# Optimization experiments

Measured on AMD Instinct MI355X. Metric: run time of the kernel, lower is better.

## Reference

```python
import jax, jax.numpy as jnp
import numpy as np


def setup_inputs() -> dict:
    key = jax.random.key(0)
    feature = jax.random.normal(key, (32, 64, 128, 128), dtype=jnp.float32)
    return {"feature": feature}


def reference(feature):
    # feature: [B, C, H, W]
    B, C, H, W = feature.shape
    mgr = feature.mean()  # global mean over all elements

    # Per-(sample, channel) argmax location; row-major first-occurrence matches
    # the original strict '>' scan.
    flat_idx = jnp.argmax(feature.reshape(B, C, H * W), axis=-1)  # [B, C]
    max_x = flat_idx // W  # row index
    max_y = flat_idx % W   # col index

    i = jnp.arange(H)
    j = jnp.arange(W)
    # squared distance from each pixel to its channel's argmax: [B, C, H, W]
    dist2 = ((max_x[:, :, None, None] - i[None, None, :, None]) ** 2
             + (max_y[:, :, None, None] - j[None, None, None, :]) ** 2)
    dist2 = dist2.astype(feature.dtype)

    f2 = feature * feature
    dis_loss = jnp.sum(f2 * dist2)

    # max over OTHER channels at each pixel: top-2 over channel axis,
    # use 2nd max only for the channel that is the (first) argmax.
    t = jnp.moveaxis(feature, 1, -1)  # [B, H, W, C]
    top2, _ = jax.lax.top_k(t, 2)    # [B, H, W, 2]
    m1 = top2[..., 0][:, None, :, :]  # [B, 1, H, W]
    m2 = top2[..., 1][:, None, :, :]
    amax_c = jnp.argmax(t, axis=-1)[:, None, :, :]  # [B, 1, H, W]
    c_ids = jnp.arange(C)[None, :, None, None]      # [1, C, 1, 1]
    max_others = jnp.where(c_ids == amax_c, m2, m1)  # [B, C, H, W]

    div_loss = jnp.sum(f2 * (max_others - mgr) ** 2)

    n = B * C * H * W
    return dis_loss / n, div_loss / n
```

## Files before the change

### kernel.cpp

```cpp
#include <hip/hip_runtime.h>

#define HW    16384
#define WDIM  128
#define CDIM  64
#define BDIM  32
#define NB1   (BDIM * CDIM)
#define NB2   ((BDIM * HW) / 512)


__global__ __launch_bounds__(256) void k1_channel(const float* __restrict__ feat,
                                                  double* __restrict__ ws) {
    const int t = threadIdx.x;
    const size_t base = (size_t)blockIdx.x * HW;
    const float4* f4 = (const float4*)(feat + base);

    float4 buf[16];
    #pragma unroll
    for (int k = 0; k < 16; ++k) buf[k] = f4[t + k * 256];

    float best = -INFINITY; int bidx = 0;
    float sf = 0.f, s0 = 0.f, si = 0.f, sj = 0.f, sq = 0.f;
    #pragma unroll
    for (int k = 0; k < 16; ++k) {
        int p = t + k * 256;
        int e = p * 4;
        int i  = e >> 7;
        int jb = e & 127;
        float x0 = buf[k].x, x1 = buf[k].y, x2 = buf[k].z, x3 = buf[k].w;
        if (x0 > best) { best = x0; bidx = e;     }
        if (x1 > best) { best = x1; bidx = e + 1; }
        if (x2 > best) { best = x2; bidx = e + 2; }
        if (x3 > best) { best = x3; bidx = e + 3; }
        float q0 = x0*x0, q1 = x1*x1, q2 = x2*x2, q3 = x3*x3;
        float qs = q0 + q1 + q2 + q3;
        sf += x0 + x1 + x2 + x3;
        s0 += qs;
        si += qs * (float)i;
        sj += q0*(float)jb + q1*(float)(jb+1) + q2*(float)(jb+2) + q3*(float)(jb+3);
        float ii = (float)(i * i);
        sq += q0*(ii + (float)( jb   * jb   ))
            + q1*(ii + (float)((jb+1)*(jb+1)))
            + q2*(ii + (float)((jb+2)*(jb+2)))
            + q3*(ii + (float)((jb+3)*(jb+3)));
    }

    __shared__ float smax[256]; __shared__ int sidx[256];
    __shared__ float rf[256], r0[256], ri[256], rj[256], rq[256];
    smax[t] = best; sidx[t] = bidx;
    rf[t] = sf; r0[t] = s0; ri[t] = si; rj[t] = sj; rq[t] = sq;
    __syncthreads();

    for (int off = 128; off > 0; off >>= 1) {
        if (t < off) {
            float vo = smax[t + off]; int io = sidx[t + off];
            if (vo > smax[t] || (vo == smax[t] && io < sidx[t])) { smax[t] = vo; sidx[t] = io; }
            rf[t] += rf[t + off]; r0[t] += r0[t + off];
            ri[t] += ri[t + off]; rj[t] += rj[t + off]; rq[t] += rq[t + off];
        }
        __syncthreads();
    }

    if (t == 0) {
        int mi = sidx[0] >> 7, mj = sidx[0] & 127;
        double T0 = r0[0], TI = ri[0], TJ = rj[0], TQ = rq[0];
        double dis = (double)(mi*mi + mj*mj) * T0 + TQ - 2.0*mi*TI - 2.0*mj*TJ;
        ws[blockIdx.x]        = (double)rf[0];
        ws[2048 + blockIdx.x] = T0;
        ws[4096 + blockIdx.x] = dis;
    }
}

__global__ __launch_bounds__(256) void k2_pixel(const float* __restrict__ feat,
                                                double* __restrict__ ws) {
    const int t = threadIdx.x;
    const int pp = blockIdx.x * 256 + t;
    const int b   = pp >> 13;
    const int hw2 = pp & 8191;
    const float2* src = (const float2*)(feat + (size_t)b * CDIM * HW) + hw2;

    float2 v[CDIM];
    #pragma unroll
    for (int c = 0; c < CDIM; ++c) v[c] = src[c * (HW / 2)];

    float m1x = -INFINITY, m2x = -INFINITY; int i1x = 0;
    float m1y = -INFINITY, m2y = -INFINITY; int i1y = 0;
    #pragma unroll
    for (int c = 0; c < CDIM; ++c) {
        float x = v[c].x, y = v[c].y;
        if (x > m1x)      { m2x = m1x; m1x = x; i1x = c; }
        else if (x > m2x) { m2x = x; }
        if (y > m1y)      { m2y = m1y; m1y = y; i1y = c; }
        else if (y > m2y) { m2y = y; }
    }

    float a1 = 0.f, a2 = 0.f;
    #pragma unroll
    for (int c = 0; c < CDIM; ++c) {
        float x = v[c].x, y = v[c].y;
        float f2x = x * x, f2y = y * y;
        float mox = (c == i1x) ? m2x : m1x;
        float moy = (c == i1y) ? m2y : m1y;
        a1 += f2x * mox * mox + f2y * moy * moy;
        a2 += f2x * mox + f2y * moy;
    }

    __shared__ float r1[256], r2[256];
    r1[t] = a1; r2[t] = a2;
    __syncthreads();
    for (int off = 128; off > 0; off >>= 1) {
        if (t < off) { r1[t] += r1[t + off]; r2[t] += r2[t + off]; }
        __syncthreads();
    }
    if (t == 0) {
        ws[6144 + blockIdx.x] = (double)r1[0];
        ws[7168 + blockIdx.x] = (double)r2[0];
    }
}

__global__ __launch_bounds__(256) void k3_final(const double* __restrict__ ws,
                                                float* __restrict__ out) {
    const int t = threadIdx.x;
    double sf = 0, s0 = 0, dis = 0, a1 = 0, a2 = 0;
    for (int i = t; i < 2048; i += 256) {
        sf  += ws[i];
        s0  += ws[2048 + i];
        dis += ws[4096 + i];
    }
    for (int i = t; i < 1024; i += 256) {
        a1 += ws[6144 + i];
        a2 += ws[7168 + i];
    }
    __shared__ double r[5][256];
    r[0][t] = sf; r[1][t] = s0; r[2][t] = dis; r[3][t] = a1; r[4][t] = a2;
    __syncthreads();
    for (int off = 128; off > 0; off >>= 1) {
        if (t < off) {
            #pragma unroll
            for (int q = 0; q < 5; ++q) r[q][t] += r[q][t + off];
        }
        __syncthreads();
    }
    if (t == 0) {
        const double n = 33554432.0;
        double mgr = r[0][0] / n;
        out[0] = (float)(r[2][0] / n);
        out[1] = (float)((r[3][0] - 2.0 * mgr * r[4][0] + mgr * mgr * r[1][0]) / n);
    }
}

extern "C" void kernel_launch(void* const* d_in, const int* in_sizes, int n_in,
                              void* d_out, int out_size, void* d_ws, size_t ws_size,
                              hipStream_t stream) {
    const float* feat = (const float*)d_in[0];
    float* out = (float*)d_out;
    double* ws = (double*)d_ws;

    k1_channel<<<NB1, 256, 0, stream>>>(feat, ws);
    k2_pixel<<<NB2, 256, 0, stream>>>(feat, ws);
    k3_final<<<1, 256, 0, stream>>>(ws, out);
}
```

Baseline: 65.27 us.

## Stream pixel pass with float4 and closed-form div-loss from top-2 and sum of squares

The per-pixel kernel no longer buffers all 64 channel values in registers and makes a second pass. It streams float4 loads once, tracking the top-2 value and the sum of squares for each pixel. The div-loss terms then come in closed form: the argmax channel uses m2, and every other channel uses m1 weighted by (sum of squares minus m1 squared). This removes the 64-entry register array and the second loop, and halves the block count. The risk is float cancellation in s2 - m1^2.

Measured after the change: 58.91 us. 9.7% less time.

```diff
diff --git a/kernel.cpp b/kernel.cpp
--- a/kernel.cpp
+++ b/kernel.cpp
@@ -5,7 +5,7 @@
 #define CDIM  64
 #define BDIM  32
 #define NB1   (BDIM * CDIM)
-#define NB2   ((BDIM * HW) / 512)
+#define NB2   ((BDIM * HW) / 1024)
 
 
 __global__ __launch_bounds__(256) void k1_channel(const float* __restrict__ feat,
@@ -73,35 +73,41 @@
 __global__ __launch_bounds__(256) void k2_pixel(const float* __restrict__ feat,
                                                 double* __restrict__ ws) {
     const int t = threadIdx.x;
-    const int pp = blockIdx.x * 256 + t;
-    const int b   = pp >> 13;
-    const int hw2 = pp & 8191;
-    const float2* src = (const float2*)(feat + (size_t)b * CDIM * HW) + hw2;
+    const int p4 = blockIdx.x * 256 + t;
+    const int b   = p4 >> 12;
+    const int hw4 = p4 & 4095;
+    const float4* src = (const float4*)(feat + (size_t)b * CDIM * HW) + hw4;
 
-    float2 v[CDIM];
-    #pragma unroll
-    for (int c = 0; c < CDIM; ++c) v[c] = src[c * (HW / 2)];
+    float m1x=-INFINITY, m2x=-INFINITY, s2x=0.f;
+    float m1y=-INFINITY, m2y=-INFINITY, s2y=0.f;
+    float m1z=-INFINITY, m2z=-INFINITY, s2z=0.f;
+    float m1w=-INFINITY, m2w=-INFINITY, s2w=0.f;
 
-    float m1x = -INFINITY, m2x = -INFINITY; int i1x = 0;
-    float m1y = -INFINITY, m2y = -INFINITY; int i1y = 0;
     #pragma unroll
     for (int c = 0; c < CDIM; ++c) {
-        float x = v[c].x, y = v[c].y;
-        if (x > m1x)      { m2x = m1x; m1x = x; i1x = c; }
-        else if (x > m2x) { m2x = x; }
-        if (y > m1y)      { m2y = m1y; m1y = y; i1y = c; }
-        else if (y > m2y) { m2y = y; }
+        float4 v = src[c * (HW / 4)];
+        if (v.x > m1x) { m2x = m1x; m1x = v.x; } else { m2x = fmaxf(m2x, v.x); }
+        if (v.y > m1y) { m2y = m1y; m1y = v.y; } else { m2y = fmaxf(m2y, v.y); }
+        if (v.z > m1z) { m2z = m1z; m1z = v.z; } else { m2z = fmaxf(m2z, v.z); }
+        if (v.w > m1w) { m2w = m1w; m1w = v.w; } else { m2w = fmaxf(m2w, v.w); }
+        s2x = fmaf(v.x, v.x, s2x);
+        s2y = fmaf(v.y, v.y, s2y);
+        s2z = fmaf(v.z, v.z, s2z);
+        s2w = fmaf(v.w, v.w, s2w);
     }
 
-    float a1 = 0.f, a2 = 0.f;
-    #pragma unroll
-    for (int c = 0; c < CDIM; ++c) {
-        float x = v[c].x, y = v[c].y;
-        float f2x = x * x, f2y = y * y;
-        float mox = (c == i1x) ? m2x : m1x;
-        float moy = (c == i1y) ? m2y : m1y;
-        a1 += f2x * mox * mox + f2y * moy * moy;
-        a2 += f2x * mox + f2y * moy;
+    float a1, a2;
+    {
+        float qx = m1x*m1x, qy = m1y*m1y, qz = m1z*m1z, qw = m1w*m1w;
+        float rx = s2x - qx, ry = s2y - qy, rz = s2z - qz, rw = s2w - qw;
+        a1 = qx*rx + m2x*m2x*qx
+           + qy*ry + m2y*m2y*qy
+           + qz*rz + m2z*m2z*qz
+           + qw*rw + m2w*m2w*qw;
+        a2 = m1x*rx + m2x*qx
+           + m1y*ry + m2y*qy
+           + m1z*rz + m2z*qz
+           + m1w*rw + m2w*qw;
     }
 
     __shared__ float r1[256], r2[256];
@@ -112,8 +118,8 @@
         __syncthreads();
     }
     if (t == 0) {
-        ws[6144 + blockIdx.x] = (double)r1[0];
-        ws[7168 + blockIdx.x] = (double)r2[0];
+        ws[6144 + blockIdx.x]       = (double)r1[0];
+        ws[6144 + NB2 + blockIdx.x] = (double)r2[0];
     }
 }
 
@@ -121,14 +127,14 @@
                                                 float* __restrict__ out) {
     const int t = threadIdx.x;
     double sf = 0, s0 = 0, dis = 0, a1 = 0, a2 = 0;
-    for (int i = t; i < 2048; i += 256) {
+    for (int i = t; i < NB1; i += 256) {
         sf  += ws[i];
         s0  += ws[2048 + i];
         dis += ws[4096 + i];
     }
-    for (int i = t; i < 1024; i += 256) {
+    for (int i = t; i < NB2; i += 256) {
         a1 += ws[6144 + i];
-        a2 += ws[7168 + i];
+        a2 += ws[6144 + NB2 + i];
     }
     __shared__ double r[5][256];
     r[0][t] = sf; r[1][t] = s0; r[2][t] = dis; r[3][t] = a1; r[4][t] = a2;
```

## Fuse channel and pixel passes into one row-tiled kernel via shared memory

Applied to the files above, without the earlier changes.

Replaces the separate per-channel and per-pixel passes, which each read the whole tensor, with one kernel that loads a (batch,row) slab of all channels into LDS and computes both the top-2 divergence terms and per-channel row partials. A second small kernel reduces the row partials per channel to find the argmax and the distance loss. The divergence term is rewritten algebraically so it no longer needs the per-pixel argmax channel index. This halves global memory reads at the cost of an extra kernel launch and more workspace traffic.

Measured after the change: 54.97 us (median of 2 runs). -15.8%, faster.

```diff
diff --git a/kernel.cpp b/kernel.cpp
--- a/kernel.cpp
+++ b/kernel.cpp
@@ -1,135 +1,180 @@
 #include <hip/hip_runtime.h>
 
-#define HW    16384
-#define WDIM  128
-#define CDIM  64
-#define BDIM  32
-#define NB1   (BDIM * CDIM)
-#define NB2   ((BDIM * HW) / 512)
-
-
-__global__ __launch_bounds__(256) void k1_channel(const float* __restrict__ feat,
-                                                  double* __restrict__ ws) {
+#define HW     16384
+#define WDIM   128
+#define HDIM   128
+#define CDIM   64
+#define BDIM   32
+#define CHUNKS 128
+#define NBF    (BDIM * CHUNKS)
+#define NBC    (BDIM * CDIM)
+
+
+#define OFF_WMAX  0
+#define OFF_WIDX  (1u << 20)
+#define OFF_WSF   (2u << 20)
+#define OFF_WS0   (3u << 20)
+#define OFF_WSJ   (4u << 20)
+#define OFF_WSQJ  (5u << 20)
+#define OFF_WA1   (6u << 20)
+#define OFF_WA2   ((6u << 20) + 32768u)
+#define OFF_K3    ((6u << 20) + 65536u)
+
+__global__ __launch_bounds__(256) void f_fused(const float* __restrict__ feat,
+                                               float* __restrict__ wmax, int* __restrict__ widx,
+                                               float* __restrict__ wsf,  float* __restrict__ ws0,
+                                               float* __restrict__ wsj,  float* __restrict__ wsqj,
+                                               double* __restrict__ wa1, double* __restrict__ wa2) {
+    __shared__ float tile[CDIM * 129];
+    __shared__ float sc2[128 * 3];
+    __shared__ float ared[128 * 2];
+    __shared__ float scb[4 * 64 * 7];
+
+    const int t  = threadIdx.x;
+    const int bf = blockIdx.x;
+    const int b  = bf >> 7, row = bf & 127;
+    const float* src = feat + (size_t)b * CDIM * HW + (size_t)row * WDIM;
+
+    float4 buf[8];
+    #pragma unroll
+    for (int k = 0; k < 8; ++k) {
+        int idx = k * 256 + t;
+        int c = idx >> 5, g = idx & 31;
+        buf[k] = *(const float4*)(src + (size_t)c * HW + g * 4);
+    }
+    #pragma unroll
+    for (int k = 0; k < 8; ++k) {
+        int idx = k * 256 + t;
+        int c = idx >> 5, g = idx & 31;
+        float* dst = &tile[c * 129 + g * 4];
+        dst[0] = buf[k].x; dst[1] = buf[k].y; dst[2] = buf[k].z; dst[3] = buf[k].w;
+    }
+    __syncthreads();
+
+    {
+        const int px = t & 127, half = t >> 7;
+        float m1 = -INFINITY, m2 = -INFINITY, s2 = 0.f;
+        #pragma unroll
+        for (int cc = 0; cc < 32; ++cc) {
+            float x = tile[(half * 32 + cc) * 129 + px];
+            if (x > m1) { m2 = m1; m1 = x; } else { m2 = fmaxf(m2, x); }
+            s2 = fmaf(x, x, s2);
+        }
+        if (half) { sc2[px * 3] = m1; sc2[px * 3 + 1] = m2; sc2[px * 3 + 2] = s2; }
+        __syncthreads();
+        if (!half) {
+            float n1 = sc2[px * 3], n2 = sc2[px * 3 + 1], s2b = sc2[px * 3 + 2];
+            float mm1 = fmaxf(m1, n1);
+            float mm2 = fmaxf(fminf(m1, n1), fmaxf(m2, n2));
+            float S2 = s2 + s2b;
+            float q = mm1 * mm1, r = S2 - q;
+            ared[px * 2]     = q * r + mm2 * mm2 * q;
+            ared[px * 2 + 1] = mm1 * r + mm2 * q;
+        }
+        __syncthreads();
+        for (int off = 64; off > 0; off >>= 1) {
+            if (t < off) {
+                ared[t * 2]     += ared[(t + off) * 2];
+                ared[t * 2 + 1] += ared[(t + off) * 2 + 1];
+            }
+            __syncthreads();
+        }
+        if (t == 0) { wa1[bf] = (double)ared[0]; wa2[bf] = (double)ared[1]; }
+    }
+
+    {
+        const int ch = t & 63, sub = t >> 6;
+        const int p0 = sub * 32;
+        float bm = -INFINITY; int bpx = 0;
+        float sf = 0.f, s0 = 0.f, sj = 0.f, sqj = 0.f;
+        #pragma unroll
+        for (int i = 0; i < 32; ++i) {
+            int p = p0 + i;
+            float x = tile[ch * 129 + p];
+            if (x > bm) { bm = x; bpx = p; }
+            sf += x;
+            float q = x * x;
+            s0 += q;
+            sj  = fmaf(q, (float)p, sj);
+            sqj = fmaf(q, (float)(p * p), sqj);
+        }
+        int o = (sub * 64 + ch) * 7;
+        scb[o] = bm; scb[o + 1] = __int_as_float(bpx);
+        scb[o + 2] = sf; scb[o + 3] = s0; scb[o + 4] = sj; scb[o + 5] = sqj;
+        __syncthreads();
+        if (t < 64) {
+            float M = -INFINITY; int P = 0;
+            float SF = 0.f, S0 = 0.f, SJ = 0.f, SQ = 0.f;
+            #pragma unroll
+            for (int s = 0; s < 4; ++s) {
+                int oo = (s * 64 + t) * 7;
+                float m = scb[oo];
+                if (m > M) { M = m; P = __float_as_int(scb[oo + 1]); }
+                SF += scb[oo + 2]; S0 += scb[oo + 3];
+                SJ += scb[oo + 4]; SQ += scb[oo + 5];
+            }
+            int out = bf * 64 + t;
+            wmax[out] = M; widx[out] = P;
+            wsf[out] = SF; ws0[out] = S0; wsj[out] = SJ; wsqj[out] = SQ;
+        }
+    }
+}
+
+__global__ __launch_bounds__(128) void k3_channel(const float* __restrict__ wmax, const int* __restrict__ widx,
+                                                  const float* __restrict__ wsf,  const float* __restrict__ ws0,
+                                                  const float* __restrict__ wsj,  const float* __restrict__ wsqj,
+                                                  double* __restrict__ k3out) {
+    const int bc = blockIdx.x;
+    const int b = bc >> 6, c = bc & 63;
     const int t = threadIdx.x;
-    const size_t base = (size_t)blockIdx.x * HW;
-    const float4* f4 = (const float4*)(feat + base);
-
-    float4 buf[16];
-    #pragma unroll
-    for (int k = 0; k < 16; ++k) buf[k] = f4[t + k * 256];
-
-    float best = -INFINITY; int bidx = 0;
-    float sf = 0.f, s0 = 0.f, si = 0.f, sj = 0.f, sq = 0.f;
-    #pragma unroll
-    for (int k = 0; k < 16; ++k) {
-        int p = t + k * 256;
-        int e = p * 4;
-        int i  = e >> 7;
-        int jb = e & 127;
-        float x0 = buf[k].x, x1 = buf[k].y, x2 = buf[k].z, x3 = buf[k].w;
-        if (x0 > best) { best = x0; bidx = e;     }
-        if (x1 > best) { best = x1; bidx = e + 1; }
-        if (x2 > best) { best = x2; bidx = e + 2; }
-        if (x3 > best) { best = x3; bidx = e + 3; }
-        float q0 = x0*x0, q1 = x1*x1, q2 = x2*x2, q3 = x3*x3;
-        float qs = q0 + q1 + q2 + q3;
-        sf += x0 + x1 + x2 + x3;
-        s0 += qs;
-        si += qs * (float)i;
-        sj += q0*(float)jb + q1*(float)(jb+1) + q2*(float)(jb+2) + q3*(float)(jb+3);
-        float ii = (float)(i * i);
-        sq += q0*(ii + (float)( jb   * jb   ))
-            + q1*(ii + (float)((jb+1)*(jb+1)))
-            + q2*(ii + (float)((jb+2)*(jb+2)))
-            + q3*(ii + (float)((jb+3)*(jb+3)));
-    }
-
-    __shared__ float smax[256]; __shared__ int sidx[256];
-    __shared__ float rf[256], r0[256], ri[256], rj[256], rq[256];
-    smax[t] = best; sidx[t] = bidx;
-    rf[t] = sf; r0[t] = s0; ri[t] = si; rj[t] = sj; rq[t] = sq;
-    __syncthreads();
-
-    for (int off = 128; off > 0; off >>= 1) {
+    const int idx = (b * 128 + t) * 64 + c;
+
+    float m = wmax[idx]; int px = widx[idx];
+    float sf = wsf[idx], s0 = ws0[idx], sj = wsj[idx], sqj = wsqj[idx];
+
+    __shared__ float rm[128]; __shared__ int rr[128]; __shared__ int rp[128];
+    rm[t] = m; rr[t] = t; rp[t] = px;
+    __syncthreads();
+    for (int off = 64; off > 0; off >>= 1) {
         if (t < off) {
-            float vo = smax[t + off]; int io = sidx[t + off];
-            if (vo > smax[t] || (vo == smax[t] && io < sidx[t])) { smax[t] = vo; sidx[t] = io; }
-            rf[t] += rf[t + off]; r0[t] += r0[t + off];
-            ri[t] += ri[t + off]; rj[t] += rj[t + off]; rq[t] += rq[t + off];
-        }
-        __syncthreads();
-    }
-
+            float mo = rm[t + off];
+            if (mo > rm[t] || (mo == rm[t] && rr[t + off] < rr[t])) {
+                rm[t] = mo; rr[t] = rr[t + off]; rp[t] = rp[t + off];
+            }
+        }
+        __syncthreads();
+    }
+    const int mi = rr[0], mj = rp[0];
+
+    double di = (double)(mi - t);
+    double disc = (di * di + (double)mj * (double)mj) * (double)s0
+                - 2.0 * (double)mj * (double)sj + (double)sqj;
+
+    __shared__ double rd[128], rsf[128], rs0[128];
+    rd[t] = disc; rsf[t] = (double)sf; rs0[t] = (double)s0;
+    __syncthreads();
+    for (int off = 64; off > 0; off >>= 1) {
+        if (t < off) { rd[t] += rd[t + off]; rsf[t] += rsf[t + off]; rs0[t] += rs0[t + off]; }
+        __syncthreads();
+    }
     if (t == 0) {
-        int mi = sidx[0] >> 7, mj = sidx[0] & 127;
-        double T0 = r0[0], TI = ri[0], TJ = rj[0], TQ = rq[0];
-        double dis = (double)(mi*mi + mj*mj) * T0 + TQ - 2.0*mi*TI - 2.0*mj*TJ;
-        ws[blockIdx.x]        = (double)rf[0];
-        ws[2048 + blockIdx.x] = T0;
-        ws[4096 + blockIdx.x] = dis;
-    }
-}
-
-__global__ __launch_bounds__(256) void k2_pixel(const float* __restrict__ feat,
-                                                double* __restrict__ ws) {
-    const int t = threadIdx.x;
-    const int pp = blockIdx.x * 256 + t;
-    const int b   = pp >> 13;
-    const int hw2 = pp & 8191;
-    const float2* src = (const float2*)(feat + (size_t)b * CDIM * HW) + hw2;
-
-    float2 v[CDIM];
-    #pragma unroll
-    for (int c = 0; c < CDIM; ++c) v[c] = src[c * (HW / 2)];
-
-    float m1x = -INFINITY, m2x = -INFINITY; int i1x = 0;
-    float m1y = -INFINITY, m2y = -INFINITY; int i1y = 0;
-    #pragma unroll
-    for (int c = 0; c < CDIM; ++c) {
-        float x = v[c].x, y = v[c].y;
-        if (x > m1x)      { m2x = m1x; m1x = x; i1x = c; }
-        else if (x > m2x) { m2x = x; }
-        if (y > m1y)      { m2y = m1y; m1y = y; i1y = c; }
-        else if (y > m2y) { m2y = y; }
-    }
-
-    float a1 = 0.f, a2 = 0.f;
-    #pragma unroll
-    for (int c = 0; c < CDIM; ++c) {
-        float x = v[c].x, y = v[c].y;
-        float f2x = x * x, f2y = y * y;
-        float mox = (c == i1x) ? m2x : m1x;
-        float moy = (c == i1y) ? m2y : m1y;
-        a1 += f2x * mox * mox + f2y * moy * moy;
-        a2 += f2x * mox + f2y * moy;
-    }
-
-    __shared__ float r1[256], r2[256];
-    r1[t] = a1; r2[t] = a2;
-    __syncthreads();
-    for (int off = 128; off > 0; off >>= 1) {
-        if (t < off) { r1[t] += r1[t + off]; r2[t] += r2[t + off]; }
-        __syncthreads();
-    }
-    if (t == 0) {
-        ws[6144 + blockIdx.x] = (double)r1[0];
-        ws[7168 + blockIdx.x] = (double)r2[0];
-    }
-}
-
-__global__ __launch_bounds__(256) void k3_final(const double* __restrict__ ws,
+        k3out[bc * 3]     = rsf[0];
+        k3out[bc * 3 + 1] = rs0[0];
+        k3out[bc * 3 + 2] = rd[0];
+    }
+}
+
+__global__ __launch_bounds__(256) void k4_final(const double* __restrict__ k3out,
+                                                const double* __restrict__ wa1,
+                                                const double* __restrict__ wa2,
                                                 float* __restrict__ out) {
     const int t = threadIdx.x;
     double sf = 0, s0 = 0, dis = 0, a1 = 0, a2 = 0;
-    for (int i = t; i < 2048; i += 256) {
-        sf  += ws[i];
-        s0  += ws[2048 + i];
-        dis += ws[4096 + i];
-    }
-    for (int i = t; i < 1024; i += 256) {
-        a1 += ws[6144 + i];
-        a2 += ws[7168 + i];
-    }
+    for (int i = t; i < NBC; i += 256) {
+        sf += k3out[i * 3]; s0 += k3out[i * 3 + 1]; dis += k3out[i * 3 + 2];
+    }
+    for (int i = t; i < NBF; i += 256) { a1 += wa1[i]; a2 += wa2[i]; }
+
     __shared__ double r[5][256];
     r[0][t] = sf; r[1][t] = s0; r[2][t] = dis; r[3][t] = a1; r[4][t] = a2;
     __syncthreads();
@@ -153,9 +198,19 @@
                               hipStream_t stream) {
     const float* feat = (const float*)d_in[0];
     float* out = (float*)d_out;
-    double* ws = (double*)d_ws;
-
-    k1_channel<<<NB1, 256, 0, stream>>>(feat, ws);
-    k2_pixel<<<NB2, 256, 0, stream>>>(feat, ws);
-    k3_final<<<1, 256, 0, stream>>>(ws, out);
-}
+    char* ws = (char*)d_ws;
+
+    float*  wmax = (float*)(ws + OFF_WMAX);
+    int*    widx = (int*)  (ws + OFF_WIDX);
+    float*  wsf  = (float*)(ws + OFF_WSF);
+    float*  ws0  = (float*)(ws + OFF_WS0);
+    float*  wsj  = (float*)(ws + OFF_WSJ);
+    float*  wsqj = (float*)(ws + OFF_WSQJ);
+    double* wa1  = (double*)(ws + OFF_WA1);
+    double* wa2  = (double*)(ws + OFF_WA2);
+    double* k3o  = (double*)(ws + OFF_K3);
+
+    f_fused<<<NBF, 256, 0, stream>>>(feat, wmax, widx, wsf, ws0, wsj, wsqj, wa1, wa2);
+    k3_channel<<<NBC, 128, 0, stream>>>(wmax, widx, wsf, ws0, wsj, wsqj, k3o);
+    k4_final<<<1, 256, 0, stream>>>(k3o, wa1, wa2, out);
+}
```
